# Optimization experiments

Measured on AMD Instinct MI355X. Metric: run time of the kernel, lower is better.

Reference implementation:

```python
import jax, jax.numpy as jnp
import numpy as np

B, N, O, C, K = 2, 384, 4, 128, 64  # batch, num_points, num_ori, num_hidden, basis_dim

def setup_inputs() -> dict:
    key = jax.random.key(0)
    ks = jax.random.split(key, 5)
    return {
        "x": jax.random.normal(ks[0], (B, N, O, C), dtype=jnp.float32),
        "kernel_basis": jax.random.normal(ks[1], (B, N, N, O, K), dtype=jnp.float32),
        "fiber_kernel_basis": jax.random.normal(ks[2], (O, O, K), dtype=jnp.float32),
        "W_spatial": jax.random.normal(ks[3], (K, C), dtype=jnp.float32) / np.sqrt(K),
        "W_rot": jax.random.normal(ks[4], (K, C), dtype=jnp.float32) / np.sqrt(K),
        "bias": jnp.zeros((C,), dtype=jnp.float32),
    }

def reference(x, kernel_basis, fiber_kernel_basis, W_spatial, W_rot, bias):
    # Dense projections (no bias), as in nn.Dense(num_hidden, use_bias=False)
    spatial_kernel = jnp.einsum('bmnok,kc->bmnoc', kernel_basis, W_spatial)   # (B,M,N,O,C)
    rot_kernel = jnp.einsum('pok,kc->poc', fiber_kernel_basis, W_rot)         # (O,O,C)
    # Spatial aggregation over source points n
    y = jnp.einsum('bnoc,bmnoc->bmoc', x, spatial_kernel)                     # (B,M,O,C)
    # Fiber (orientation) aggregation over o
    y = jnp.einsum('bmoc,poc->bmpc', y, rot_kernel)                           # (B,M,O,C)
    return y + bias
```

## Files before the change

kernel.cpp:

```cpp
#include <hip/hip_runtime.h>

typedef __attribute__((ext_vector_type(4)))  float    f32x4;
typedef __attribute__((ext_vector_type(16))) float    f32x16;
typedef __attribute__((ext_vector_type(8)))  _Float16 f16x8;

#define NB 2
#define NN 384
#define NO 4
#define NC 128
#define NK 64
#define MT 128
#define NMT 3

__device__ __forceinline__ void async16(const float* g, float* l) {
    __builtin_amdgcn_global_load_lds((const __attribute__((address_space(1))) void*)g,
                                     (__attribute__((address_space(3))) void*)l, 16, 0, 0);
}

__global__ __launch_bounds__(256, 2)
void sepconv_stage1(const float* __restrict__ KB, const float* __restrict__ X,
                    const float* __restrict__ Ws, float* __restrict__ part,
                    int ns)
{
    extern __shared__ float smem[];
    float* Abuf = smem;
    float* xlds = smem + 4 * 2 * 2048;

    const int t    = threadIdx.x;
    const int lane = t & 63;
    const int w    = t >> 6;
    const int l31  = lane & 31;
    const int half = lane >> 5;

    const int wg    = blockIdx.x;
    const int b     = wg & 1;
    const int o     = (wg >> 1) & 3;
    const int mt    = (wg >> 3) % NMT;
    const int split = wg / 24;
    const int n0    = split * ns;

    f16x8 wsreg[4][4];
    {
        const float* wp = Ws + half * 8 * NC + l31;
#pragma unroll
        for (int cs = 0; cs < 4; ++cs)
#pragma unroll
            for (int kc = 0; kc < 4; ++kc) {
                f16x8 v;
#pragma unroll
                for (int j = 0; j < 8; ++j)
                    v[j] = (_Float16)wp[(kc * 16 + j) * NC + cs * 32];
                wsreg[cs][kc] = v;
            }
    }

    for (int idx = t; idx < ns * NC; idx += 256) {
        const int nl = idx >> 7, c = idx & 127;
        xlds[idx] = X[((b * NN + n0 + nl) * NO + o) * NC + c];
    }
    __syncthreads();

    const int mrow = mt * MT + w * 32 + l31;
    const float* gbase = KB + (size_t)(b * NN + mrow) * (NN * NO * NK)
                            + (size_t)n0 * (NO * NK) + o * NK + half * 4;
    float* const wbuf = Abuf + w * 2 * 2048;

    auto stage = [&](int nl, int p) {
        const float* g = gbase + (size_t)nl * (NO * NK);
        float* l = wbuf + p * 2048;
#pragma unroll
        for (int i = 0; i < 8; ++i)
            async16(g + i * 8, l + i * 256);
    };

    f32x16 acc[4];
#pragma unroll
    for (int cs = 0; cs < 4; ++cs)
#pragma unroll
        for (int r = 0; r < 16; ++r) acc[cs][r] = 0.f;

    stage(0, 0);
    stage(1, 1);

    for (int i = 0; i < ns; ++i) {
        if (i < ns - 1) __builtin_amdgcn_s_waitcnt(0x0F78);
        else            __builtin_amdgcn_s_waitcnt(0x0F70);
        __builtin_amdgcn_sched_barrier(0);

        f16x8 xh[4];
#pragma unroll
        for (int cs = 0; cs < 4; ++cs) {
            const _Float16 xv = (_Float16)xlds[i * NC + cs * 32 + l31];
            f16x8 s;
#pragma unroll
            for (int j = 0; j < 8; ++j) s[j] = xv;
            xh[cs] = s;
        }

        const float* ab = wbuf + (i & 1) * 2048 + half * 256 + l31 * 4;
#pragma unroll
        for (int kc = 0; kc < 4; ++kc) {
            const f32x4 a0 = *(const f32x4*)(ab + kc * 512);
            const f32x4 a1 = *(const f32x4*)(ab + kc * 512 + 128);
            f16x8 af;
#pragma unroll
            for (int j = 0; j < 4; ++j) { af[j] = (_Float16)a0[j]; af[4 + j] = (_Float16)a1[j]; }
#pragma unroll
            for (int cs = 0; cs < 4; ++cs) {
                const f16x8 bf = xh[cs] * wsreg[cs][kc];
                acc[cs] = __builtin_amdgcn_mfma_f32_32x32x16_f16(af, bf, acc[cs], 0, 0, 0);
            }
        }

        __builtin_amdgcn_sched_barrier(0);
        if (i + 2 < ns) stage(i + 2, i & 1);
    }

    float* pb = part + ((size_t)(split * NB + b) * NO + o) * (NN * NC)
                     + (mt * MT + w * 32) * NC;
#pragma unroll
    for (int cs = 0; cs < 4; ++cs)
#pragma unroll
        for (int r = 0; r < 16; ++r) {
            const int ml = (r & 3) + 8 * (r >> 2) + 4 * half;
            pb[ml * NC + cs * 32 + l31] = acc[cs][r];
        }
}

__global__ __launch_bounds__(256)
void sepconv_stage2(const float* __restrict__ part, const float* __restrict__ fiber,
                    const float* __restrict__ Wr, const float* __restrict__ bias,
                    float* __restrict__ out, int nsplit)
{
    const int bid = blockIdx.x;
    const int b = bid / NN;
    const int m = bid % NN;
    const int t = threadIdx.x;
    const int c = t & 127;
    const int g = t >> 7;

    float rot[8];
#pragma unroll
    for (int i = 0; i < 8; ++i) rot[i] = 0.f;
    for (int k = 0; k < NK; ++k) {
        const float wv = Wr[k * NC + c];
#pragma unroll
        for (int q = 0; q < 2; ++q)
#pragma unroll
            for (int oo = 0; oo < 4; ++oo)
                rot[q * 4 + oo] += fiber[((2 * g + q) * NO + oo) * NK + k] * wv;
    }

    float y1[4];
#pragma unroll
    for (int oo = 0; oo < 4; ++oo) {
        float s = 0.f;
        for (int sp = 0; sp < nsplit; ++sp)
            s += part[((size_t)(sp * NB + b) * NO + oo) * (NN * NC) + m * NC + c];
        y1[oo] = s;
    }

    const float bv = bias[c];
#pragma unroll
    for (int q = 0; q < 2; ++q) {
        float v = bv;
#pragma unroll
        for (int oo = 0; oo < 4; ++oo) v += y1[oo] * rot[q * 4 + oo];
        out[((b * NN + m) * NO + (2 * g + q)) * NC + c] = v;
    }
}

extern "C" void kernel_launch(void* const* d_in, const int* in_sizes, int n_in,
                              void* d_out, int out_size, void* d_ws, size_t ws_size,
                              hipStream_t stream)
{
    const float* X    = (const float*)d_in[0];
    const float* KB   = (const float*)d_in[1];
    const float* FB   = (const float*)d_in[2];
    const float* Ws   = (const float*)d_in[3];
    const float* Wr   = (const float*)d_in[4];
    const float* bias = (const float*)d_in[5];
    float* out  = (float*)d_out;
    float* part = (float*)d_ws;

    const size_t per = (size_t)NB * NO * NN * NC * sizeof(float);
    int nsplit = 16;
    if (ws_size >= 32 * per) {  }
    while (nsplit > 16 && (size_t)nsplit * per > ws_size) nsplit >>= 1;
    const int ns = NN / nsplit;

    const size_t lds = (4 * 2 * 2048 + (size_t)ns * NC) * sizeof(float);

    sepconv_stage1<<<dim3(24 * nsplit), dim3(256), lds, stream>>>(KB, X, Ws, part, ns);
    sepconv_stage2<<<dim3(NB * NN), dim3(256), 0, stream>>>(part, FB, Wr, bias, out, nsplit);
}
```

Measured before the change: 491.7 us.

## Re-tile stage1 over channel-split waves with a three-deep swizzled LDS pipeline

Stage1 is reorganised so each workgroup covers 32 m-rows and two orientations, and each wave owns a 32-channel slice instead of 32 m-rows with all four channel slices. Kernel-basis rows are loaded into LDS with a lane-rotated swizzle to avoid bank conflicts, through a three-slot ring buffer that uses workgroup barriers in place of per-wave double buffering. The fp32-to-fp16 conversion now uses packed cvt_pkrtz, and the grid grows from 384 to 768 blocks. The aim is better occupancy and latency hiding for the memory-bound kernel-basis stream, at the cost of more barriers and less reuse of each loaded A tile per wave.

```diff
diff --git a/kernel.cpp b/kernel.cpp
--- a/kernel.cpp
+++ b/kernel.cpp
@@ -1,5 +1,6 @@
 #include <hip/hip_runtime.h>
 
+typedef __attribute__((ext_vector_type(2)))  __fp16   pk16x2;
 typedef __attribute__((ext_vector_type(4)))  float    f32x4;
 typedef __attribute__((ext_vector_type(16))) float    f32x16;
 typedef __attribute__((ext_vector_type(8)))  _Float16 f16x8;
@@ -9,8 +10,14 @@
 #define NO 4
 #define NC 128
 #define NK 64
-#define MT 128
-#define NMT 3
+#define MTW 32
+#define NSPLIT 16
+#define NS (NN / NSPLIT)
+#define DEPTH 3
+#define SLOTF 4096
+#define SLOTB 16384
+
+union F16x8u { f16x8 v; pk16x2 h[4]; };
 
 __device__ __forceinline__ void async16(const float* g, float* l) {
     __builtin_amdgcn_global_load_lds((const __attribute__((address_space(1))) void*)g,
@@ -19,111 +26,134 @@
 
 __global__ __launch_bounds__(256, 2)
 void sepconv_stage1(const float* __restrict__ KB, const float* __restrict__ X,
-                    const float* __restrict__ Ws, float* __restrict__ part,
-                    int ns)
+                    const float* __restrict__ Ws, float* __restrict__ part)
 {
     extern __shared__ float smem[];
     float* Abuf = smem;
-    float* xlds = smem + 4 * 2 * 2048;
+    float* xlds = smem + DEPTH * SLOTF;
 
     const int t    = threadIdx.x;
     const int lane = t & 63;
     const int w    = t >> 6;
     const int l31  = lane & 31;
-    const int half = lane >> 5;
-
-    const int wg    = blockIdx.x;
-    const int b     = wg & 1;
-    const int o     = (wg >> 1) & 3;
-    const int mt    = (wg >> 3) % NMT;
-    const int split = wg / 24;
-    const int n0    = split * ns;
-
-    f16x8 wsreg[4][4];
+    const int lh   = lane >> 5;
+
+    const int bid   = blockIdx.x;
+    const int mt    = bid % 12;
+    const int p     = (bid / 12) & 1;
+    const int b     = (bid / 24) & 1;
+    const int split = bid / 48;
+    const int n0    = split * NS;
+    const int cidx  = w * 32 + l31;
+
+    f16x8 wsreg[4];
     {
-        const float* wp = Ws + half * 8 * NC + l31;
-#pragma unroll
-        for (int cs = 0; cs < 4; ++cs)
+        const float* wp = Ws + (lh * 8) * NC + cidx;
+#pragma unroll
+        for (int kc = 0; kc < 4; ++kc) {
+            f16x8 v;
+#pragma unroll
+            for (int j = 0; j < 8; ++j)
+                v[j] = (_Float16)wp[(kc * 16 + j) * NC];
+            wsreg[kc] = v;
+        }
+    }
+
+    for (int idx = t; idx < NS * 256; idx += 256) {
+        const int nl = idx >> 8, rest = idx & 255;
+        xlds[idx] = X[((b * NN + n0 + nl) * NO + 2 * p + (rest >> 7)) * NC + (rest & 127)];
+    }
+    __syncthreads();
+
+    const float* gb[4];
+#pragma unroll
+    for (int j = 0; j < 4; ++j) {
+        const int r = 8 * w + 2 * j + lh;
+        const int m = mt * MTW + r;
+        gb[j] = KB + ((size_t)(b * NN + m) * NN + n0) * (NO * NK)
+                   + p * (2 * NK) + (((l31 + r) & 31) << 2);
+    }
+
+    int apos[2][4][2];
+#pragma unroll
+    for (int o = 0; o < 2; ++o)
+#pragma unroll
+        for (int kc = 0; kc < 4; ++kc) {
+            const int q0 = o * 16 + kc * 4 + lh * 2;
+            apos[o][kc][0] = l31 * 512 + ((q0     - l31) & 31) * 16;
+            apos[o][kc][1] = l31 * 512 + ((q0 + 1 - l31) & 31) * 16;
+        }
+
+    f32x16 acc[2];
+#pragma unroll
+    for (int o = 0; o < 2; ++o)
+#pragma unroll
+        for (int r = 0; r < 16; ++r) acc[o][r] = 0.f;
+
+    auto stage = [&](int nl, int slot) {
+        float* lb = Abuf + slot * SLOTF + w * 1024;
+#pragma unroll
+        for (int j = 0; j < 4; ++j)
+            async16(gb[j] + nl * (NO * NK), lb + j * 256);
+    };
+
+    auto compute = [&](int i, int slot) {
+        const char* sb = (const char*)Abuf + slot * SLOTB;
+#pragma unroll
+        for (int o = 0; o < 2; ++o) {
+            const _Float16 xv = (_Float16)xlds[i * 256 + o * 128 + cidx];
+            f16x8 xh;
+#pragma unroll
+            for (int j = 0; j < 8; ++j) xh[j] = xv;
 #pragma unroll
             for (int kc = 0; kc < 4; ++kc) {
-                f16x8 v;
-#pragma unroll
-                for (int j = 0; j < 8; ++j)
-                    v[j] = (_Float16)wp[(kc * 16 + j) * NC + cs * 32];
-                wsreg[cs][kc] = v;
+                const f32x4 a0 = *(const f32x4*)(sb + apos[o][kc][0]);
+                const f32x4 a1 = *(const f32x4*)(sb + apos[o][kc][1]);
+                F16x8u af;
+                af.h[0] = __builtin_amdgcn_cvt_pkrtz(a0[0], a0[1]);
+                af.h[1] = __builtin_amdgcn_cvt_pkrtz(a0[2], a0[3]);
+                af.h[2] = __builtin_amdgcn_cvt_pkrtz(a1[0], a1[1]);
+                af.h[3] = __builtin_amdgcn_cvt_pkrtz(a1[2], a1[3]);
+                const f16x8 bf = xh * wsreg[kc];
+                acc[o] = __builtin_amdgcn_mfma_f32_32x32x16_f16(af.v, bf, acc[o], 0, 0, 0);
             }
-    }
-
-    for (int idx = t; idx < ns * NC; idx += 256) {
-        const int nl = idx >> 7, c = idx & 127;
-        xlds[idx] = X[((b * NN + n0 + nl) * NO + o) * NC + c];
-    }
-    __syncthreads();
-
-    const int mrow = mt * MT + w * 32 + l31;
-    const float* gbase = KB + (size_t)(b * NN + mrow) * (NN * NO * NK)
-                            + (size_t)n0 * (NO * NK) + o * NK + half * 4;
-    float* const wbuf = Abuf + w * 2 * 2048;
-
-    auto stage = [&](int nl, int p) {
-        const float* g = gbase + (size_t)nl * (NO * NK);
-        float* l = wbuf + p * 2048;
-#pragma unroll
-        for (int i = 0; i < 8; ++i)
-            async16(g + i * 8, l + i * 256);
+        }
     };
-
-    f32x16 acc[4];
-#pragma unroll
-    for (int cs = 0; cs < 4; ++cs)
-#pragma unroll
-        for (int r = 0; r < 16; ++r) acc[cs][r] = 0.f;
 
     stage(0, 0);
     stage(1, 1);
 
-    for (int i = 0; i < ns; ++i) {
-        if (i < ns - 1) __builtin_amdgcn_s_waitcnt(0x0F78);
-        else            __builtin_amdgcn_s_waitcnt(0x0F70);
-        __builtin_amdgcn_sched_barrier(0);
-
-        f16x8 xh[4];
-#pragma unroll
-        for (int cs = 0; cs < 4; ++cs) {
-            const _Float16 xv = (_Float16)xlds[i * NC + cs * 32 + l31];
-            f16x8 s;
-#pragma unroll
-            for (int j = 0; j < 8; ++j) s[j] = xv;
-            xh[cs] = s;
-        }
-
-        const float* ab = wbuf + (i & 1) * 2048 + half * 256 + l31 * 4;
-#pragma unroll
-        for (int kc = 0; kc < 4; ++kc) {
-            const f32x4 a0 = *(const f32x4*)(ab + kc * 512);
-            const f32x4 a1 = *(const f32x4*)(ab + kc * 512 + 128);
-            f16x8 af;
-#pragma unroll
-            for (int j = 0; j < 4; ++j) { af[j] = (_Float16)a0[j]; af[4 + j] = (_Float16)a1[j]; }
-#pragma unroll
-            for (int cs = 0; cs < 4; ++cs) {
-                const f16x8 bf = xh[cs] * wsreg[cs][kc];
-                acc[cs] = __builtin_amdgcn_mfma_f32_32x32x16_f16(af, bf, acc[cs], 0, 0, 0);
-            }
-        }
-
-        __builtin_amdgcn_sched_barrier(0);
-        if (i + 2 < ns) stage(i + 2, i & 1);
-    }
-
-    float* pb = part + ((size_t)(split * NB + b) * NO + o) * (NN * NC)
-                     + (mt * MT + w * 32) * NC;
-#pragma unroll
-    for (int cs = 0; cs < 4; ++cs)
+    for (int ii = 0; ii + DEPTH < NS; ii += DEPTH) {
+#pragma unroll
+        for (int s = 0; s < DEPTH; ++s) {
+            __builtin_amdgcn_s_waitcnt(0x0F74);
+            __builtin_amdgcn_s_barrier();
+            __builtin_amdgcn_sched_barrier(0);
+            stage(ii + s + 2, (s + 2) % 3);
+            __builtin_amdgcn_sched_barrier(0);
+            compute(ii + s, s);
+        }
+    }
+    __builtin_amdgcn_s_waitcnt(0x0F74); __builtin_amdgcn_s_barrier();
+    __builtin_amdgcn_sched_barrier(0);
+    stage(NS - 1, 2);
+    __builtin_amdgcn_sched_barrier(0);
+    compute(NS - 3, 0);
+    __builtin_amdgcn_s_waitcnt(0x0F74); __builtin_amdgcn_s_barrier();
+    __builtin_amdgcn_sched_barrier(0);
+    compute(NS - 2, 1);
+    __builtin_amdgcn_s_waitcnt(0x0F70); __builtin_amdgcn_s_barrier();
+    __builtin_amdgcn_sched_barrier(0);
+    compute(NS - 1, 2);
+
+    float* pb = part + ((size_t)(split * NB + b) * NO + 2 * p) * (NN * NC)
+                     + (size_t)(mt * MTW) * NC + cidx;
+#pragma unroll
+    for (int o = 0; o < 2; ++o)
 #pragma unroll
         for (int r = 0; r < 16; ++r) {
-            const int ml = (r & 3) + 8 * (r >> 2) + 4 * half;
-            pb[ml * NC + cs * 32 + l31] = acc[cs][r];
+            const int ml = (r & 3) + 8 * (r >> 2) + 4 * lh;
+            pb[(size_t)o * NN * NC + ml * NC] = acc[o][r];
         }
 }
 
@@ -183,14 +213,8 @@
     float* out  = (float*)d_out;
     float* part = (float*)d_ws;
 
-    const size_t per = (size_t)NB * NO * NN * NC * sizeof(float);
-    int nsplit = 16;
-    if (ws_size >= 32 * per) {  }
-    while (nsplit > 16 && (size_t)nsplit * per > ws_size) nsplit >>= 1;
-    const int ns = NN / nsplit;
-
-    const size_t lds = (4 * 2 * 2048 + (size_t)ns * NC) * sizeof(float);
-
-    sepconv_stage1<<<dim3(24 * nsplit), dim3(256), lds, stream>>>(KB, X, Ws, part, ns);
-    sepconv_stage2<<<dim3(NB * NN), dim3(256), 0, stream>>>(part, FB, Wr, bias, out, nsplit);
-}
+    const size_t lds = (DEPTH * SLOTF + NS * 256) * sizeof(float);
+
+    sepconv_stage1<<<dim3(12 * 2 * NB * NSPLIT), dim3(256), lds, stream>>>(KB, X, Ws, part);
+    sepconv_stage2<<<dim3(NB * NN), dim3(256), 0, stream>>>(part, FB, Wr, bias, out, NSPLIT);
+}
```

Result: faster. 451.8 us (-8.1%).
